# Optimization experiments

Measured on AMD Instinct MI355X. Metric: run time of the kernel, lower is better.

The kernel has to match this reference:

```python
import jax, jax.numpy as jnp
import numpy as np

B, S, I, H, O, F = 8192, 100, 15, 128, 2, 30  # batch, seq, input, hidden, out, future


def _lstm_cell(x, h, c, w_ih, w_hh, b):
    # PyTorch gate order: input, forget, cell(g), output
    gates = x @ w_ih.T + h @ w_hh.T + b  # [B, 4H]
    i, f, g, o = jnp.split(gates, 4, axis=-1)
    c2 = jax.nn.sigmoid(f) * c + jax.nn.sigmoid(i) * jnp.tanh(g)
    h2 = jax.nn.sigmoid(o) * jnp.tanh(c2)
    return h2, c2


def setup_inputs() -> dict:
    key = jax.random.key(0)
    ks = jax.random.split(key, 12)
    s = 1.0 / np.sqrt(H)  # PyTorch LSTM/Linear init scale
    u = lambda k, shape: jax.random.uniform(k, shape, jnp.float32, -s, s)
    return {
        "x": jax.random.normal(ks[0], (B, S, I), jnp.float32),
        "w_ih0": u(ks[1], (4 * H, I)),
        "w_hh0": u(ks[2], (4 * H, H)),
        "b_ih0": u(ks[3], (4 * H,)),
        "b_hh0": u(ks[4], (4 * H,)),
        "w_ih1": u(ks[5], (4 * H, H)),
        "w_hh1": u(ks[6], (4 * H, H)),
        "b_ih1": u(ks[7], (4 * H,)),
        "b_hh1": u(ks[8], (4 * H,)),
        "fc_w": u(ks[9], (O, H)),
        "fc_b": u(ks[10], (O,)),
        "future_frames": F,
    }


def reference(x, w_ih0, w_hh0, b_ih0, b_hh0, w_ih1, w_hh1, b_ih1, b_hh1, fc_w, fc_b, future_frames):
    bsz = x.shape[0]
    hid = w_hh0.shape[1]
    b0 = b_ih0 + b_hh0
    b1 = b_ih1 + b_hh1

    # ---- encoder: run full 2-layer LSTM over the observed sequence ----
    xs = jnp.transpose(x, (1, 0, 2))  # [S, B, I]
    z = jnp.zeros((bsz, hid), x.dtype)

    def enc_step(carry, xt):
        h0, c0, h1, c1 = carry
        h0, c0 = _lstm_cell(xt, h0, c0, w_ih0, w_hh0, b0)
        h1, c1 = _lstm_cell(h0, h1, c1, w_ih1, w_hh1, b1)
        return (h0, c0, h1, c1), None

    (h0, c0, h1, c1), _ = jax.lax.scan(enc_step, (z, z, z, z), xs)

    def dec_step(carry, _):
        h0, c0, h1, c1, inp = carry
        h0, c0 = _lstm_cell(inp, h0, c0, w_ih0, w_hh0, b0)
        h1, c1 = _lstm_cell(h0, h1, c1, w_ih1, w_hh1, b1)
        pred = h1 @ fc_w.T + fc_b  # [B, 2]
        nxt = inp.at[:, :2].set(pred)
        return (h0, c0, h1, c1, nxt), pred

    _, preds = jax.lax.scan(dec_step, (h0, c0, h1, c1, x[:, -1, :]), None, length=future_frames)
    return jnp.transpose(preds, (1, 0, 2))  # [B, future_frames, 2]
```

## Files before the change

kernel.cpp:

```cpp
#include <hip/hip_runtime.h>


typedef _Float16 half_t;
typedef _Float16 half8 __attribute__((ext_vector_type(8)));
typedef _Float16 half4 __attribute__((ext_vector_type(4)));
typedef float f32x4 __attribute__((ext_vector_type(4)));

#define SEQ 100
#define FUT 30
#define TOT (SEQ + FUT)
#define NIN 15
#define MB  16
#define L2E 1.44269504f

#define MFMA32(A, B, C) __builtin_amdgcn_mfma_f32_16x16x32_f16((A), (B), (C), 0, 0, 0)
#define MFMA16(A, B, C) __builtin_amdgcn_mfma_f32_16x16x16f16((A), (B), (C), 0, 0, 0)

__global__ void prep_kernel(const float* __restrict__ w_ih0, const float* __restrict__ w_hh0,
                            const float* __restrict__ b_ih0, const float* __restrict__ b_hh0,
                            const float* __restrict__ w_ih1, const float* __restrict__ w_hh1,
                            const float* __restrict__ b_ih1, const float* __restrict__ b_hh1,
                            half_t* __restrict__ wsh)
{
  int idx = blockIdx.x * 256 + threadIdx.x;
  if (idx < 196608) {
    int seg = idx >> 16;
    int r   = idx & 65535;
    int n   = r >> 7, k = r & 127;
    int g   = (n >> 4) & 3;
    int row = g * 128 + ((n >> 6) << 4) + (n & 15);
    float sc = (g == 2) ? (2.0f * L2E) : (-L2E);
    const float* src = (seg == 0) ? w_hh0 : ((seg == 1) ? w_ih1 : w_hh1);
    wsh[idx] = (half_t)(src[row * 128 + k] * sc);
  } else if (idx < 204800) {
    int r   = idx - 196608;
    int n   = r >> 4, k = r & 15;
    int g   = (n >> 4) & 3;
    int row = g * 128 + ((n >> 6) << 4) + (n & 15);
    float sc = (g == 2) ? (2.0f * L2E) : (-L2E);
    wsh[idx] = (half_t)((k < NIN) ? (w_ih0[row * NIN + k] * sc) : 0.0f);
  } else if (idx < 205824) {
    int r     = idx - 204800;
    float* bv = (float*)(wsh + 204800);
    int which = r >> 9, n = r & 511;
    int g     = (n >> 4) & 3;
    int row   = g * 128 + ((n >> 6) << 4) + (n & 15);
    float sc  = (g == 2) ? (2.0f * L2E) : (-L2E);
    bv[r] = ((which == 0) ? (b_ih0[row] + b_hh0[row]) : (b_ih1[row] + b_hh1[row])) * sc;
  }
}

__global__ __launch_bounds__(512, 2)
void lstm_kernel(const float* __restrict__ x,
                 const half_t* __restrict__ wsh,
                 const float* __restrict__ fcw,
                 const float* __restrict__ fcb,
                 float* __restrict__ out)
{
  __shared__ __align__(16) half_t sx[SEQ * MB * 16];
  __shared__ __align__(16) half_t sh0[2][MB * 128];
  __shared__ __align__(16) half_t sh1[2][MB * 128];
  __shared__ __align__(16) half_t swx[512 * 16];
  __shared__ __align__(16) half_t sdec[MB * 16];
  __shared__ __align__(16) float  sbias[1024];
  __shared__ __align__(16) float  sfc[258];

  const half_t* WH0 = wsh;
  const half_t* WI1 = wsh + 65536;
  const half_t* WH1 = wsh + 131072;
  const half_t* WX  = wsh + 196608;
  const float*  BV  = (const float*)(wsh + 204800);

  const int tid   = threadIdx.x;
  const int wave  = tid >> 6;
  const int lane  = tid & 63;
  const int l16   = lane & 15;
  const int quad  = lane >> 4;
  const int nb    = wave * 64;
  const int bbase = blockIdx.x * MB;

  half8 wh0[4][4], wi1[4][4], wh1[4][4];
  #pragma unroll
  for (int kt = 0; kt < 4; ++kt) {
    #pragma unroll
    for (int g = 0; g < 4; ++g) {
      int n = nb + g * 16 + l16;
      int k = kt * 32 + quad * 8;
      wh0[kt][g] = *(const half8*)&WH0[n * 128 + k];
      wi1[kt][g] = *(const half8*)&WI1[n * 128 + k];
      wh1[kt][g] = *(const half8*)&WH1[n * 128 + k];
    }
  }

  for (int it = tid; it < MB * SEQ * NIN; it += 512) {
    int b = it / (SEQ * NIN); int r = it - b * (SEQ * NIN);
    int s = r / NIN;          int i = r - s * NIN;
    sx[(s * MB + b) * 16 + i] = (half_t)x[(size_t)(bbase + b) * (SEQ * NIN) + r];
  }
  for (int it = tid; it < SEQ * MB; it += 512) sx[it * 16 + 15] = (half_t)0;
  for (int it = tid; it < 8192; it += 512)     swx[it] = WX[it];
  for (int it = tid; it < 1024; it += 512)     sbias[it] = BV[it];
  if (tid < 256) sfc[tid] = fcw[tid];
  if (tid < 2)   sfc[256 + tid] = fcb[tid];
  if (tid < 256) {
    int b = tid >> 4, i = tid & 15;
    sdec[tid] = (i < NIN) ? (half_t)x[(size_t)(bbase + b) * (SEQ * NIN) + 99 * NIN + i]
                          : (half_t)0;
  }
  for (int it = tid; it < MB * 128; it += 512) {
    sh0[0][it] = (half_t)0; sh0[1][it] = (half_t)0;
    sh1[0][it] = (half_t)0; sh1[1][it] = (half_t)0;
  }
  __syncthreads();

  float c0[4] = {0.f, 0.f, 0.f, 0.f};
  float c1[4] = {0.f, 0.f, 0.f, 0.f};
  const int chunk = wave * 2 + (l16 >> 3);

  #define ACT_STORE(ACC, CS, DST)                                              \
    _Pragma("unroll")                                                          \
    for (int r = 0; r < 4; ++r) {                                              \
      float A  = __builtin_amdgcn_exp2f((ACC)[0][r]);                          \
      float C  = __builtin_amdgcn_exp2f((ACC)[1][r]);                          \
      float B  = __builtin_amdgcn_exp2f((ACC)[2][r]);                          \
      float D  = __builtin_amdgcn_exp2f((ACC)[3][r]);                          \
      float oA = 1.f + A, oB = 1.f + B, oC = 1.f + C, oD = 1.f + D;            \
      float P  = oA * oB;                                                      \
      float t  = (B - 1.f) * oC;                                               \
      float nm = fmaf((CS)[r], P, t);                                          \
      float rc = __builtin_amdgcn_rcpf(P * oC);                                \
      float cn = nm * rc;                                                      \
      (CS)[r] = cn;                                                            \
      float E  = __builtin_amdgcn_exp2f(2.0f * L2E * cn);                      \
      float h  = (E - 1.f) * __builtin_amdgcn_rcpf(oD * (1.f + E));            \
      int   m  = quad * 4 + r;                                                 \
      (DST)[m * 128 + ((chunk ^ (m & 7)) << 3) + (l16 & 7)] = (half_t)h;       \
    }

  int cur = 0;
  for (int s = 0; s < TOT; ++s) {
    const int nxt = cur ^ 1;
    const half_t* xsrc = (s < SEQ) ? &sx[s * MB * 16] : sdec;

    {
      f32x4 acc[4];
      #pragma unroll
      for (int g = 0; g < 4; ++g) {
        float b = sbias[nb + g * 16 + l16];
        acc[g] = (f32x4){b, b, b, b};
      }
      #pragma unroll
      for (int kt = 0; kt < 4; ++kt) {
        int c = kt * 4 + quad;
        half8 ah = *(const half8*)&sh0[cur][l16 * 128 + ((c ^ (l16 & 7)) << 3)];
        #pragma unroll
        for (int g = 0; g < 4; ++g) acc[g] = MFMA32(ah, wh0[kt][g], acc[g]);
      }
      half4 ax = *(const half4*)&xsrc[l16 * 16 + quad * 4];
      #pragma unroll
      for (int g = 0; g < 4; ++g) {
        half4 bx = *(const half4*)&swx[(nb + g * 16 + l16) * 16 + quad * 4];
        acc[g] = MFMA16(ax, bx, acc[g]);
      }
      ACT_STORE(acc, c0, sh0[nxt])
    }
    __syncthreads();

    {
      f32x4 acc[4];
      #pragma unroll
      for (int g = 0; g < 4; ++g) {
        float b = sbias[512 + nb + g * 16 + l16];
        acc[g] = (f32x4){b, b, b, b};
      }
      #pragma unroll
      for (int kt = 0; kt < 4; ++kt) {
        int c = kt * 4 + quad;
        half8 ah = *(const half8*)&sh0[nxt][l16 * 128 + ((c ^ (l16 & 7)) << 3)];
        #pragma unroll
        for (int g = 0; g < 4; ++g) acc[g] = MFMA32(ah, wi1[kt][g], acc[g]);
      }
      #pragma unroll
      for (int kt = 0; kt < 4; ++kt) {
        int c = kt * 4 + quad;
        half8 ah = *(const half8*)&sh1[cur][l16 * 128 + ((c ^ (l16 & 7)) << 3)];
        #pragma unroll
        for (int g = 0; g < 4; ++g) acc[g] = MFMA32(ah, wh1[kt][g], acc[g]);
      }
      ACT_STORE(acc, c1, sh1[nxt])
    }

    if (s >= SEQ) {
      __syncthreads();
      if (tid < 256) {
        int b   = wave * 4 + (lane >> 4);
        int o   = (lane >> 3) & 1;
        int seg = lane & 7;
        float p = 0.f;
        #pragma unroll
        for (int cc = 0; cc < 2; ++cc) {
          int c = seg * 2 + cc;
          half8 hv = *(const half8*)&sh1[nxt][b * 128 + ((c ^ (b & 7)) << 3)];
          f32x4 w0 = *(const f32x4*)&sfc[o * 128 + c * 8];
          f32x4 w1 = *(const f32x4*)&sfc[o * 128 + c * 8 + 4];
          #pragma unroll
          for (int u = 0; u < 4; ++u) p = fmaf((float)hv[u], w0[u], p);
          #pragma unroll
          for (int u = 0; u < 4; ++u) p = fmaf((float)hv[4 + u], w1[u], p);
        }
        p += __shfl_down(p, 4);
        p += __shfl_down(p, 2);
        p += __shfl_down(p, 1);
        if (seg == 0) {
          p += sfc[256 + o];
          out[(size_t)(bbase + b) * (FUT * 2) + (s - SEQ) * 2 + o] = p;
          sdec[b * 16 + o] = (half_t)p;
        }
      }
      __syncthreads();
    }

    cur = nxt;
  }
}

extern "C" void kernel_launch(void* const* d_in, const int* in_sizes, int n_in,
                              void* d_out, int out_size, void* d_ws, size_t ws_size,
                              hipStream_t stream)
{
  (void)in_sizes; (void)n_in; (void)out_size; (void)ws_size;
  const float* x     = (const float*)d_in[0];
  const float* w_ih0 = (const float*)d_in[1];
  const float* w_hh0 = (const float*)d_in[2];
  const float* b_ih0 = (const float*)d_in[3];
  const float* b_hh0 = (const float*)d_in[4];
  const float* w_ih1 = (const float*)d_in[5];
  const float* w_hh1 = (const float*)d_in[6];
  const float* b_ih1 = (const float*)d_in[7];
  const float* b_hh1 = (const float*)d_in[8];
  const float* fcw   = (const float*)d_in[9];
  const float* fcb   = (const float*)d_in[10];
  float*  out = (float*)d_out;
  half_t* wsh = (half_t*)d_ws;

  prep_kernel<<<(205824 + 255) / 256, 256, 0, stream>>>(
      w_ih0, w_hh0, b_ih0, b_hh0, w_ih1, w_hh1, b_ih1, b_hh1, wsh);
  lstm_kernel<<<8192 / MB, 512, 0, stream>>>(x, wsh, fcw, fcb, out);
}
```

Measured before the change: 634.6 us.

## Keep input weights in registers, re-layout x staging, and refine LDS swizzle

Moves the per-wave slice of the input-projection weights from shared memory into registers, which removes four LDS reads per timestep. The staged x (and the decoder input) is re-laid out as [s][k/4][b][4] so each quad's half4 load is contiguous, and the x load loop now writes the padding zero directly. The hidden-state XOR swizzle also folds in bit 3 of the row index to avoid bank conflicts between rows 0-7 and 8-15. The trade-off is a few more VGPRs under the 512-thread, 2-blocks-per-CU launch bound, and a smaller LDS footprint.

```diff
diff --git a/kernel.cpp b/kernel.cpp
--- a/kernel.cpp
+++ b/kernel.cpp
@@ -57,11 +57,10 @@
                  const float* __restrict__ fcb,
                  float* __restrict__ out)
 {
-  __shared__ __align__(16) half_t sx[SEQ * MB * 16];
+  __shared__ __align__(16) half_t sx[SEQ * 4 * MB * 4];
   __shared__ __align__(16) half_t sh0[2][MB * 128];
   __shared__ __align__(16) half_t sh1[2][MB * 128];
-  __shared__ __align__(16) half_t swx[512 * 16];
-  __shared__ __align__(16) half_t sdec[MB * 16];
+  __shared__ __align__(16) half_t sdec[4 * MB * 4];
   __shared__ __align__(16) float  sbias[1024];
   __shared__ __align__(16) float  sfc[258];
 
@@ -91,21 +90,25 @@
       wh1[kt][g] = *(const half8*)&WH1[n * 128 + k];
     }
   }
-
-  for (int it = tid; it < MB * SEQ * NIN; it += 512) {
-    int b = it / (SEQ * NIN); int r = it - b * (SEQ * NIN);
-    int s = r / NIN;          int i = r - s * NIN;
-    sx[(s * MB + b) * 16 + i] = (half_t)x[(size_t)(bbase + b) * (SEQ * NIN) + r];
-  }
-  for (int it = tid; it < SEQ * MB; it += 512) sx[it * 16 + 15] = (half_t)0;
-  for (int it = tid; it < 8192; it += 512)     swx[it] = WX[it];
-  for (int it = tid; it < 1024; it += 512)     sbias[it] = BV[it];
+  half4 wxr[4];
+  #pragma unroll
+  for (int g = 0; g < 4; ++g)
+    wxr[g] = *(const half4*)&WX[(nb + g * 16 + l16) * 16 + quad * 4];
+
+  for (int it = tid; it < SEQ * MB * 16; it += 512) {
+    int s = it >> 8;
+    int rem = it & 255;
+    int b = rem >> 4, i = rem & 15;
+    float v = (i < NIN) ? x[(size_t)(bbase + b) * (SEQ * NIN) + s * NIN + i] : 0.f;
+    sx[((s * 4 + (i >> 2)) * MB + b) * 4 + (i & 3)] = (half_t)v;
+  }
+  for (int it = tid; it < 1024; it += 512) sbias[it] = BV[it];
   if (tid < 256) sfc[tid] = fcw[tid];
   if (tid < 2)   sfc[256 + tid] = fcb[tid];
   if (tid < 256) {
     int b = tid >> 4, i = tid & 15;
-    sdec[tid] = (i < NIN) ? (half_t)x[(size_t)(bbase + b) * (SEQ * NIN) + 99 * NIN + i]
-                          : (half_t)0;
+    float v = (i < NIN) ? x[(size_t)(bbase + b) * (SEQ * NIN) + 99 * NIN + i] : 0.f;
+    sdec[((i >> 2) * MB + b) * 4 + (i & 3)] = (half_t)v;
   }
   for (int it = tid; it < MB * 128; it += 512) {
     sh0[0][it] = (half_t)0; sh0[1][it] = (half_t)0;
@@ -115,7 +118,8 @@
 
   float c0[4] = {0.f, 0.f, 0.f, 0.f};
   float c1[4] = {0.f, 0.f, 0.f, 0.f};
-  const int chunk = wave * 2 + (l16 >> 3);
+  const int kc    = wave * 2 + (l16 >> 3);
+  const int vread = (l16 & 7) ^ ((l16 >> 3) << 1);
 
   #define ACT_STORE(ACC, CS, DST)                                              \
     _Pragma("unroll")                                                          \
@@ -134,13 +138,14 @@
       float E  = __builtin_amdgcn_exp2f(2.0f * L2E * cn);                      \
       float h  = (E - 1.f) * __builtin_amdgcn_rcpf(oD * (1.f + E));            \
       int   m  = quad * 4 + r;                                                 \
-      (DST)[m * 128 + ((chunk ^ (m & 7)) << 3) + (l16 & 7)] = (half_t)h;       \
+      int   vm = (m & 7) ^ ((m >> 3) << 1);                                    \
+      (DST)[m * 128 + ((kc ^ vm) << 3) + (l16 & 7)] = (half_t)h;               \
     }
 
   int cur = 0;
   for (int s = 0; s < TOT; ++s) {
     const int nxt = cur ^ 1;
-    const half_t* xsrc = (s < SEQ) ? &sx[s * MB * 16] : sdec;
+    const half_t* xsrc = (s < SEQ) ? &sx[s * 4 * MB * 4] : sdec;
 
     {
       f32x4 acc[4];
@@ -152,16 +157,13 @@
       #pragma unroll
       for (int kt = 0; kt < 4; ++kt) {
         int c = kt * 4 + quad;
-        half8 ah = *(const half8*)&sh0[cur][l16 * 128 + ((c ^ (l16 & 7)) << 3)];
+        half8 ah = *(const half8*)&sh0[cur][l16 * 128 + ((c ^ vread) << 3)];
         #pragma unroll
         for (int g = 0; g < 4; ++g) acc[g] = MFMA32(ah, wh0[kt][g], acc[g]);
       }
-      half4 ax = *(const half4*)&xsrc[l16 * 16 + quad * 4];
-      #pragma unroll
-      for (int g = 0; g < 4; ++g) {
-        half4 bx = *(const half4*)&swx[(nb + g * 16 + l16) * 16 + quad * 4];
-        acc[g] = MFMA16(ax, bx, acc[g]);
-      }
+      half4 ax = *(const half4*)&xsrc[(quad * MB + l16) * 4];
+      #pragma unroll
+      for (int g = 0; g < 4; ++g) acc[g] = MFMA16(ax, wxr[g], acc[g]);
       ACT_STORE(acc, c0, sh0[nxt])
     }
     __syncthreads();
@@ -176,14 +178,14 @@
       #pragma unroll
       for (int kt = 0; kt < 4; ++kt) {
         int c = kt * 4 + quad;
-        half8 ah = *(const half8*)&sh0[nxt][l16 * 128 + ((c ^ (l16 & 7)) << 3)];
+        half8 ah = *(const half8*)&sh0[nxt][l16 * 128 + ((c ^ vread) << 3)];
         #pragma unroll
         for (int g = 0; g < 4; ++g) acc[g] = MFMA32(ah, wi1[kt][g], acc[g]);
       }
       #pragma unroll
       for (int kt = 0; kt < 4; ++kt) {
         int c = kt * 4 + quad;
-        half8 ah = *(const half8*)&sh1[cur][l16 * 128 + ((c ^ (l16 & 7)) << 3)];
+        half8 ah = *(const half8*)&sh1[cur][l16 * 128 + ((c ^ vread) << 3)];
         #pragma unroll
         for (int g = 0; g < 4; ++g) acc[g] = MFMA32(ah, wh1[kt][g], acc[g]);
       }
@@ -196,11 +198,12 @@
         int b   = wave * 4 + (lane >> 4);
         int o   = (lane >> 3) & 1;
         int seg = lane & 7;
+        int vb  = (b & 7) ^ ((b >> 3) << 1);
         float p = 0.f;
         #pragma unroll
         for (int cc = 0; cc < 2; ++cc) {
           int c = seg * 2 + cc;
-          half8 hv = *(const half8*)&sh1[nxt][b * 128 + ((c ^ (b & 7)) << 3)];
+          half8 hv = *(const half8*)&sh1[nxt][b * 128 + ((c ^ vb) << 3)];
           f32x4 w0 = *(const f32x4*)&sfc[o * 128 + c * 8];
           f32x4 w1 = *(const f32x4*)&sfc[o * 128 + c * 8 + 4];
           #pragma unroll
@@ -214,7 +217,7 @@
         if (seg == 0) {
           p += sfc[256 + o];
           out[(size_t)(bbase + b) * (FUT * 2) + (s - SEQ) * 2 + o] = p;
-          sdec[b * 16 + o] = (half_t)p;
+          sdec[b * 4 + o] = (half_t)p;
         }
       }
       __syncthreads();
```

After: 655.3 us. 3.3% more time.

## Process two 16-row batch tiles per block and stream x from global with prefetch

Applied to the files above, without the earlier changes.

Each block now handles two independent 16-row batch tiles, interleaving their layer computations so that MFMA and activation work from one tile can overlap with the other while sharing the register-resident weights and the per-step barriers. The shared-memory staging of the whole x sequence is removed; instead each lane loads its float4 slice of x directly from global memory one step ahead and converts it to an fp16 fragment in registers. This halves the grid to 256 blocks, and on a large-CU device that may leave compute units underused. It also doubles the per-step serial work inside each block and adds global-load latency to the recurrent loop.

```diff
diff --git a/kernel.cpp b/kernel.cpp
--- a/kernel.cpp
+++ b/kernel.cpp
@@ -50,6 +50,14 @@
   }
 }
 
+__device__ __forceinline__ half4 xfrag(float4 v, int quad) {
+  float a = (quad < 3) ? v.x : v.y;
+  float b = (quad < 3) ? v.y : v.z;
+  float c = (quad < 3) ? v.z : v.w;
+  float d = (quad < 3) ? v.w : 0.0f;
+  return (half4){(half_t)a, (half_t)b, (half_t)c, (half_t)d};
+}
+
 __global__ __launch_bounds__(512, 2)
 void lstm_kernel(const float* __restrict__ x,
                  const half_t* __restrict__ wsh,
@@ -57,11 +65,10 @@
                  const float* __restrict__ fcb,
                  float* __restrict__ out)
 {
-  __shared__ __align__(16) half_t sx[SEQ * MB * 16];
-  __shared__ __align__(16) half_t sh0[2][MB * 128];
-  __shared__ __align__(16) half_t sh1[2][MB * 128];
-  __shared__ __align__(16) half_t swx[512 * 16];
-  __shared__ __align__(16) half_t sdec[MB * 16];
+  __shared__ __align__(16) half_t sh0[2][2][MB * 128];
+  __shared__ __align__(16) half_t sh1[2][2][MB * 128];
+  __shared__ __align__(16) half_t swx[8192];
+  __shared__ __align__(16) half_t sdec[2][MB * 16];
   __shared__ __align__(16) float  sbias[1024];
   __shared__ __align__(16) float  sfc[258];
 
@@ -77,7 +84,7 @@
   const int l16   = lane & 15;
   const int quad  = lane >> 4;
   const int nb    = wave * 64;
-  const int bbase = blockIdx.x * MB;
+  const int bbase = blockIdx.x * (2 * MB);
 
   half8 wh0[4][4], wi1[4][4], wh1[4][4];
   #pragma unroll
@@ -92,29 +99,25 @@
     }
   }
 
-  for (int it = tid; it < MB * SEQ * NIN; it += 512) {
-    int b = it / (SEQ * NIN); int r = it - b * (SEQ * NIN);
-    int s = r / NIN;          int i = r - s * NIN;
-    sx[(s * MB + b) * 16 + i] = (half_t)x[(size_t)(bbase + b) * (SEQ * NIN) + r];
-  }
-  for (int it = tid; it < SEQ * MB; it += 512) sx[it * 16 + 15] = (half_t)0;
-  for (int it = tid; it < 8192; it += 512)     swx[it] = WX[it];
-  for (int it = tid; it < 1024; it += 512)     sbias[it] = BV[it];
+  for (int it = tid; it < 8192; it += 512) swx[it] = WX[it];
+  for (int it = tid; it < 1024; it += 512) sbias[it] = BV[it];
   if (tid < 256) sfc[tid] = fcw[tid];
   if (tid < 2)   sfc[256 + tid] = fcb[tid];
-  if (tid < 256) {
+  {
     int b = tid >> 4, i = tid & 15;
-    sdec[tid] = (i < NIN) ? (half_t)x[(size_t)(bbase + b) * (SEQ * NIN) + 99 * NIN + i]
-                          : (half_t)0;
+    float v = (i < NIN) ? x[(size_t)(bbase + b) * (SEQ * NIN) + 99 * NIN + i] : 0.f;
+    sdec[b >> 4][(b & 15) * 16 + i] = (half_t)v;
   }
   for (int it = tid; it < MB * 128; it += 512) {
-    sh0[0][it] = (half_t)0; sh0[1][it] = (half_t)0;
-    sh1[0][it] = (half_t)0; sh1[1][it] = (half_t)0;
+    sh0[0][0][it] = (half_t)0; sh0[0][1][it] = (half_t)0;
+    sh0[1][0][it] = (half_t)0; sh0[1][1][it] = (half_t)0;
+    sh1[0][0][it] = (half_t)0; sh1[0][1][it] = (half_t)0;
+    sh1[1][0][it] = (half_t)0; sh1[1][1][it] = (half_t)0;
   }
   __syncthreads();
 
-  float c0[4] = {0.f, 0.f, 0.f, 0.f};
-  float c1[4] = {0.f, 0.f, 0.f, 0.f};
+  float c0A[4] = {0.f, 0.f, 0.f, 0.f}, c0B[4] = {0.f, 0.f, 0.f, 0.f};
+  float c1A[4] = {0.f, 0.f, 0.f, 0.f}, c1B[4] = {0.f, 0.f, 0.f, 0.f};
   const int chunk = wave * 2 + (l16 >> 3);
 
   #define ACT_STORE(ACC, CS, DST)                                              \
@@ -137,70 +140,103 @@
       (DST)[m * 128 + ((chunk ^ (m & 7)) << 3) + (l16 & 7)] = (half_t)h;       \
     }
 
+  #define P0_SEC(T, AX, CS)                                                    \
+    {                                                                          \
+      f32x4 acc[4];                                                            \
+      _Pragma("unroll")                                                        \
+      for (int g = 0; g < 4; ++g) {                                            \
+        float b = sbias[nb + g * 16 + l16];                                    \
+        acc[g] = (f32x4){b, b, b, b};                                          \
+      }                                                                        \
+      _Pragma("unroll")                                                        \
+      for (int kt = 0; kt < 4; ++kt) {                                         \
+        int c = kt * 4 + quad;                                                 \
+        half8 ah = *(const half8*)&sh0[T][cur][l16 * 128 + ((c ^ (l16 & 7)) << 3)]; \
+        _Pragma("unroll")                                                      \
+        for (int g = 0; g < 4; ++g) acc[g] = MFMA32(ah, wh0[kt][g], acc[g]);   \
+      }                                                                        \
+      _Pragma("unroll")                                                        \
+      for (int g = 0; g < 4; ++g) {                                            \
+        half4 bx = *(const half4*)&swx[(nb + g * 16 + l16) * 16 + quad * 4];   \
+        acc[g] = MFMA16((AX), bx, acc[g]);                                     \
+      }                                                                        \
+      ACT_STORE(acc, CS, (&sh0[T][nxt][0]))                                    \
+    }
+
+  #define P1_SEC(T, CS)                                                        \
+    {                                                                          \
+      f32x4 acc[4];                                                            \
+      _Pragma("unroll")                                                        \
+      for (int g = 0; g < 4; ++g) {                                            \
+        float b = sbias[512 + nb + g * 16 + l16];                              \
+        acc[g] = (f32x4){b, b, b, b};                                          \
+      }                                                                        \
+      _Pragma("unroll")                                                        \
+      for (int kt = 0; kt < 4; ++kt) {                                         \
+        int c = kt * 4 + quad;                                                 \
+        half8 ah = *(const half8*)&sh0[T][nxt][l16 * 128 + ((c ^ (l16 & 7)) << 3)]; \
+        _Pragma("unroll")                                                      \
+        for (int g = 0; g < 4; ++g) acc[g] = MFMA32(ah, wi1[kt][g], acc[g]);   \
+      }                                                                        \
+      _Pragma("unroll")                                                        \
+      for (int kt = 0; kt < 4; ++kt) {                                         \
+        int c = kt * 4 + quad;                                                 \
+        half8 ah = *(const half8*)&sh1[T][cur][l16 * 128 + ((c ^ (l16 & 7)) << 3)]; \
+        _Pragma("unroll")                                                      \
+        for (int g = 0; g < 4; ++g) acc[g] = MFMA32(ah, wh1[kt][g], acc[g]);   \
+      }                                                                        \
+      ACT_STORE(acc, CS, (&sh1[T][nxt][0]))                                    \
+    }
+
+  const int koff = (quad < 3) ? quad * 4 : 11;
+  const float* xpA = x + (size_t)(bbase + l16) * (SEQ * NIN) + koff;
+  const float* xpB = xpA + (size_t)MB * (SEQ * NIN);
+  float4 xfA = *(const float4*)xpA;
+  float4 xfB = *(const float4*)xpB;
+  xpA += NIN; xpB += NIN;
+
   int cur = 0;
   for (int s = 0; s < TOT; ++s) {
     const int nxt = cur ^ 1;
-    const half_t* xsrc = (s < SEQ) ? &sx[s * MB * 16] : sdec;
-
-    {
-      f32x4 acc[4];
-      #pragma unroll
-      for (int g = 0; g < 4; ++g) {
-        float b = sbias[nb + g * 16 + l16];
-        acc[g] = (f32x4){b, b, b, b};
-      }
-      #pragma unroll
-      for (int kt = 0; kt < 4; ++kt) {
-        int c = kt * 4 + quad;
-        half8 ah = *(const half8*)&sh0[cur][l16 * 128 + ((c ^ (l16 & 7)) << 3)];
-        #pragma unroll
-        for (int g = 0; g < 4; ++g) acc[g] = MFMA32(ah, wh0[kt][g], acc[g]);
-      }
-      half4 ax = *(const half4*)&xsrc[l16 * 16 + quad * 4];
-      #pragma unroll
-      for (int g = 0; g < 4; ++g) {
-        half4 bx = *(const half4*)&swx[(nb + g * 16 + l16) * 16 + quad * 4];
-        acc[g] = MFMA16(ax, bx, acc[g]);
-      }
-      ACT_STORE(acc, c0, sh0[nxt])
-    }
+
+    float4 xnA = xfA, xnB = xfB;
+    const bool pf = (s + 1 < SEQ);
+    if (pf) {
+      xnA = *(const float4*)xpA;
+      xnB = *(const float4*)xpB;
+      xpA += NIN; xpB += NIN;
+    }
+
+    half4 axA, axB;
+    if (s < SEQ) {
+      axA = xfrag(xfA, quad);
+      axB = xfrag(xfB, quad);
+    } else {
+      axA = *(const half4*)&sdec[0][l16 * 16 + quad * 4];
+      axB = *(const half4*)&sdec[1][l16 * 16 + quad * 4];
+    }
+
+    P0_SEC(0, axA, c0A)
+    __builtin_amdgcn_sched_barrier(0);
+    P0_SEC(1, axB, c0B)
     __syncthreads();
 
-    {
-      f32x4 acc[4];
-      #pragma unroll
-      for (int g = 0; g < 4; ++g) {
-        float b = sbias[512 + nb + g * 16 + l16];
-        acc[g] = (f32x4){b, b, b, b};
-      }
-      #pragma unroll
-      for (int kt = 0; kt < 4; ++kt) {
-        int c = kt * 4 + quad;
-        half8 ah = *(const half8*)&sh0[nxt][l16 * 128 + ((c ^ (l16 & 7)) << 3)];
-        #pragma unroll
-        for (int g = 0; g < 4; ++g) acc[g] = MFMA32(ah, wi1[kt][g], acc[g]);
-      }
-      #pragma unroll
-      for (int kt = 0; kt < 4; ++kt) {
-        int c = kt * 4 + quad;
-        half8 ah = *(const half8*)&sh1[cur][l16 * 128 + ((c ^ (l16 & 7)) << 3)];
-        #pragma unroll
-        for (int g = 0; g < 4; ++g) acc[g] = MFMA32(ah, wh1[kt][g], acc[g]);
-      }
-      ACT_STORE(acc, c1, sh1[nxt])
-    }
+    P1_SEC(0, c1A)
+    __builtin_amdgcn_sched_barrier(0);
+    P1_SEC(1, c1B)
 
     if (s >= SEQ) {
       __syncthreads();
-      if (tid < 256) {
+      {
         int b   = wave * 4 + (lane >> 4);
+        int tl  = b >> 4, row = b & 15;
         int o   = (lane >> 3) & 1;
         int seg = lane & 7;
         float p = 0.f;
         #pragma unroll
         for (int cc = 0; cc < 2; ++cc) {
           int c = seg * 2 + cc;
-          half8 hv = *(const half8*)&sh1[nxt][b * 128 + ((c ^ (b & 7)) << 3)];
+          half8 hv = *(const half8*)&sh1[tl][nxt][row * 128 + ((c ^ (row & 7)) << 3)];
           f32x4 w0 = *(const f32x4*)&sfc[o * 128 + c * 8];
           f32x4 w1 = *(const f32x4*)&sfc[o * 128 + c * 8 + 4];
           #pragma unroll
@@ -214,12 +250,13 @@
         if (seg == 0) {
           p += sfc[256 + o];
           out[(size_t)(bbase + b) * (FUT * 2) + (s - SEQ) * 2 + o] = p;
-          sdec[b * 16 + o] = (half_t)p;
+          sdec[tl][row * 16 + o] = (half_t)p;
         }
       }
       __syncthreads();
     }
 
+    xfA = xnA; xfB = xnB;
     cur = nxt;
   }
 }
@@ -245,5 +282,5 @@
 
   prep_kernel<<<(205824 + 255) / 256, 256, 0, stream>>>(
       w_ih0, w_hh0, b_ih0, b_hh0, w_ih1, w_hh1, b_ih1, b_hh1, wsh);
-  lstm_kernel<<<8192 / MB, 512, 0, stream>>>(x, wsh, fcw, fcb, out);
-}
+  lstm_kernel<<<8192 / (2 * MB), 512, 0, stream>>>(x, wsh, fcw, fcb, out);
+}
```

New measurement: 890.2 us. 40.3% more time.
